# Kernel tuning notes

Hardware: AMD Instinct MI355X
Metric: run time of the kernel (lower is better)

Reference implementation:

```python
import jax, jax.numpy as jnp
import numpy as np

N_NODES = 100000
N_EDGES = 1600000
IN_DIM = 128
HID = 64
N_GRAPHS = 1024
EPS = 1e-5


def setup_inputs() -> dict:
    key = jax.random.key(0)
    ks = jax.random.split(key, 16)
    x = jax.random.normal(ks[0], (N_NODES, IN_DIM), dtype=jnp.float32)
    edge_index = jax.random.randint(ks[1], (2, N_EDGES), 0, N_NODES, dtype=jnp.int32)
    batch = jnp.sort(jax.random.randint(ks[2], (N_NODES,), 0, N_GRAPHS, dtype=jnp.int32))
    def glorot(k, shape):
        lim = np.sqrt(6.0 / (shape[0] + shape[1]))
        return jax.random.uniform(k, shape, jnp.float32, -lim, lim)
    return {
        'x': x, 'edge_index': edge_index, 'batch': batch,
        'w1': glorot(ks[3], (IN_DIM, HID)), 'b1': jnp.zeros((HID,), jnp.float32),
        'g1': jnp.ones((HID,), jnp.float32), 'be1': jnp.zeros((HID,), jnp.float32),
        'w2': glorot(ks[4], (HID, HID)), 'b2': jnp.zeros((HID,), jnp.float32),
        'g2': jnp.ones((HID,), jnp.float32), 'be2': jnp.zeros((HID,), jnp.float32),
        'w3': glorot(ks[5], (HID, HID)), 'b3': jnp.zeros((HID,), jnp.float32),
        'g3': jnp.ones((HID,), jnp.float32), 'be3': jnp.zeros((HID,), jnp.float32),
        'fc_w': glorot(ks[6], (HID, 1)), 'fc_b': jnp.zeros((1,), jnp.float32),
    }


def _batch_norm(h, gamma, beta):
    # training-mode BN over the node dimension (biased variance, as torch)
    mean = jnp.mean(h, axis=0)
    var = jnp.mean((h - mean) ** 2, axis=0)
    return (h - mean) * jax.lax.rsqrt(var + EPS) * gamma + beta


def reference(x, edge_index, batch, w1, b1, g1, be1, w2, b2, g2, be2,
              w3, b3, g3, be3, fc_w, fc_b):
    n = x.shape[0]
    # GCN normalization with added self-loops (PyG GCNConv semantics)
    loop = jnp.arange(n, dtype=edge_index.dtype)
    row = jnp.concatenate([edge_index[0], loop])  # source
    col = jnp.concatenate([edge_index[1], loop])  # target
    deg = jax.ops.segment_sum(jnp.ones_like(col, dtype=x.dtype), col, num_segments=n)
    dinv = jnp.where(deg > 0, jax.lax.rsqrt(deg), 0.0)
    norm = (dinv[row] * dinv[col])[:, None]  # [E+N, 1]

    def gcn(h, W, b):
        m = h @ W                                   # [N, HID]
        agg = jax.ops.segment_sum(m[row] * norm, col, num_segments=n)
        return agg + b

    h = jax.nn.relu(_batch_norm(gcn(x, w1, b1), g1, be1))
    res = h  # dropout is identity in eval mode
    h = jax.nn.relu(_batch_norm(gcn(h, w2, b2), g2, be2) + res)
    h = jax.nn.relu(_batch_norm(gcn(h, w3, b3), g3, be3))

    # global mean pool over graphs
    sums = jax.ops.segment_sum(h, batch, num_segments=N_GRAPHS)
    cnt = jax.ops.segment_sum(jnp.ones((n,), x.dtype), batch, num_segments=N_GRAPHS)
    pooled = sums / jnp.maximum(cnt, 1.0)[:, None]
    return (pooled @ fc_w + fc_b).squeeze(-1)  # [N_GRAPHS]
```

## Files before the change

kernel.cpp:

```cpp
#include <hip/hip_runtime.h>

#define NN 100000
#define NE 1600000
#define INDIM 128
#define HID 64
#define NG 1024
#define NB 1563
#define SCB 256
#define EPB ((NE + SCB - 1) / SCB)
#define SEGCAP 2048
#define BN_EPS 1e-5f

typedef unsigned short u16;
typedef unsigned int u32;

__device__ __forceinline__ u16 f2bf(float f) {
    u32 u = __float_as_uint(f);
    u32 r = (u + 0x7fffu + ((u >> 16) & 1u)) >> 16;
    return (u16)r;
}
__device__ __forceinline__ float bf2f(u32 b) {
    return __uint_as_float(b << 16);
}


__global__ void k_hist(const int* __restrict__ col, int* __restrict__ hist, int E) {
    __shared__ int h[NB];
    int b = blockIdx.x;
    for (int i = threadIdx.x; i < NB; i += 256) h[i] = 0;
    __syncthreads();
    int s = b * EPB, e = min(s + EPB, E);
    for (int i = s + threadIdx.x; i < e; i += 256) {
        atomicAdd(&h[col[i] >> 6], 1);
    }
    __syncthreads();
    for (int i = threadIdx.x; i < NB; i += 256) hist[b * NB + i] = h[i];
}

__global__ void k_btot(const int* __restrict__ hist, int* __restrict__ bcnt) {
    int t = blockIdx.x * 256 + threadIdx.x;
    if (t < NB) {
        int s = 0;
        for (int b = 0; b < SCB; b++) s += hist[b * NB + t];
        bcnt[t] = s;
    }
}

__global__ void k_bscan(const int* __restrict__ bcnt, int* __restrict__ bstart, int B, int E) {
    __shared__ int ts[256];
    int t = threadIdx.x;
    int loc[7];
    int s = 0;
    for (int i = 0; i < 7; i++) {
        int idx = t * 7 + i;
        loc[i] = (idx < B) ? bcnt[idx] : 0;
        s += loc[i];
    }
    ts[t] = s;
    __syncthreads();
    for (int off = 1; off < 256; off <<= 1) {
        int add = (t >= off) ? ts[t - off] : 0;
        __syncthreads();
        ts[t] += add;
        __syncthreads();
    }
    int ex = ts[t] - s;
    for (int i = 0; i < 7; i++) {
        int idx = t * 7 + i;
        if (idx < B) bstart[idx] = ex;
        ex += loc[i];
    }
    if (t == 0) bstart[B] = E;
}

__global__ void k_hcol(int* __restrict__ hist, const int* __restrict__ bstart) {
    int t = blockIdx.x * 256 + threadIdx.x;
    if (t < NB) {
        int run = bstart[t];
        for (int b = 0; b < SCB; b++) {
            int idx = b * NB + t;
            int v = hist[idx];
            hist[idx] = run;
            run += v;
        }
    }
}

__global__ void k_scatter(const int* __restrict__ row, const int* __restrict__ col,
                          const int* __restrict__ hist, u32* __restrict__ ebuf, int E) {
    __shared__ int cur[NB];
    int b = blockIdx.x;
    for (int i = threadIdx.x; i < NB; i += 256) cur[i] = hist[b * NB + i];
    __syncthreads();
    int s = b * EPB, e = min(s + EPB, E);
    for (int i = s + threadIdx.x; i < e; i += 256) {
        int c = col[i];
        int p = atomicAdd(&cur[c >> 6], 1);
        ebuf[p] = ((u32)row[i] << 6) | (u32)(c & 63);
    }
}

__global__ void k_degb(const u32* __restrict__ ebuf, const int* __restrict__ bstart,
                       float* __restrict__ dinv, int N) {
    __shared__ int lcnt[64];
    int b = blockIdx.x, t = threadIdx.x;
    if (t < 64) lcnt[t] = 0;
    __syncthreads();
    int s = bstart[b], e = bstart[b + 1];
    for (int i = s + t; i < e; i += 256) {
        atomicAdd(&lcnt[ebuf[i] & 63u], 1);
    }
    __syncthreads();
    if (t < 64) {
        int node = b * 64 + t;
        if (node < N) dinv[node] = rsqrtf((float)(lcnt[t] + 1));
    }
}


template<int K>
__global__ void k_gemm(const float* __restrict__ h, const float* __restrict__ W,
                       const float* __restrict__ dinv, u16* __restrict__ m, int N,
                       const float* __restrict__ bnStats, const float* __restrict__ bnG,
                       const float* __restrict__ bnB) {
    __shared__ float sh[16][K];
    const float invN = 1.0f / (float)N;
    const int K4 = K / 4;
    int block0 = blockIdx.x * 16;
    for (int idx = threadIdx.x; idx < 16 * K4; idx += 256) {
        int nn = idx / K4, kk4 = idx % K4;
        int node = block0 + nn;
        float4 v = make_float4(0.f, 0.f, 0.f, 0.f);
        if (node < N) v = *(const float4*)(h + (size_t)node * K + kk4 * 4);
        if (bnStats) {
            #pragma unroll
            for (int j = 0; j < 4; j++) {
                int kk = kk4 * 4 + j;
                float mean = bnStats[kk] * invN;
                float var = bnStats[K + kk] * invN - mean * mean;
                float sc = bnG[kk] * rsqrtf(var + BN_EPS);
                float* pv = (j == 0) ? &v.x : (j == 1) ? &v.y : (j == 2) ? &v.z : &v.w;
                *pv = fmaxf((*pv - mean) * sc + bnB[kk], 0.f);
            }
        }
        *(float4*)(&sh[nn][kk4 * 4]) = v;
    }
    __syncthreads();
    int colj = threadIdx.x & 63;
    int nl = threadIdx.x >> 6;
    float a0 = 0.f, a1 = 0.f, a2 = 0.f, a3 = 0.f;
    #pragma unroll 8
    for (int k = 0; k < K; k++) {
        float w = W[k * HID + colj];
        a0 += sh[nl][k] * w;
        a1 += sh[nl + 4][k] * w;
        a2 += sh[nl + 8][k] * w;
        a3 += sh[nl + 12][k] * w;
    }
    int n0 = block0 + nl;
    if (n0 < N)      m[(size_t)n0 * HID + colj]        = f2bf(a0 * dinv[n0]);
    if (n0 + 4 < N)  m[(size_t)(n0 + 4) * HID + colj]  = f2bf(a1 * dinv[n0 + 4]);
    if (n0 + 8 < N)  m[(size_t)(n0 + 8) * HID + colj]  = f2bf(a2 * dinv[n0 + 8]);
    if (n0 + 12 < N) m[(size_t)(n0 + 12) * HID + colj] = f2bf(a3 * dinv[n0 + 12]);
}

__global__ void k_gemm3(const float* __restrict__ agg1, const float* __restrict__ agg2,
                        const float* __restrict__ st1, const float* __restrict__ st2,
                        const float* __restrict__ g1, const float* __restrict__ be1,
                        const float* __restrict__ g2, const float* __restrict__ be2,
                        const float* __restrict__ W, const float* __restrict__ dinv,
                        u16* __restrict__ m, int N) {
    __shared__ float sh[16][HID];
    const float invN = 1.0f / (float)N;
    int block0 = blockIdx.x * 16;
    for (int idx = threadIdx.x; idx < 16 * 16; idx += 256) {
        int nn = idx / 16, kk4 = idx % 16;
        int node = block0 + nn;
        float4 o = make_float4(0.f, 0.f, 0.f, 0.f);
        if (node < N) {
            size_t p = (size_t)node * HID + kk4 * 4;
            float4 v1 = *(const float4*)(agg1 + p);
            float4 v2 = *(const float4*)(agg2 + p);
            float* p1 = &v1.x; float* p2 = &v2.x; float* po = &o.x;
            #pragma unroll
            for (int j = 0; j < 4; j++) {
                int kk = kk4 * 4 + j;
                float m1 = st1[kk] * invN;
                float va1 = st1[64 + kk] * invN - m1 * m1;
                float s1 = g1[kk] * rsqrtf(va1 + BN_EPS);
                float h1 = fmaxf((p1[j] - m1) * s1 + be1[kk], 0.f);
                float m2 = st2[kk] * invN;
                float va2 = st2[64 + kk] * invN - m2 * m2;
                float s2 = g2[kk] * rsqrtf(va2 + BN_EPS);
                po[j] = fmaxf((p2[j] - m2) * s2 + be2[kk] + h1, 0.f);
            }
        }
        *(float4*)(&sh[nn][kk4 * 4]) = o;
    }
    __syncthreads();
    int colj = threadIdx.x & 63;
    int nl = threadIdx.x >> 6;
    float a0 = 0.f, a1 = 0.f, a2 = 0.f, a3 = 0.f;
    #pragma unroll 8
    for (int k = 0; k < HID; k++) {
        float w = W[k * HID + colj];
        a0 += sh[nl][k] * w;
        a1 += sh[nl + 4][k] * w;
        a2 += sh[nl + 8][k] * w;
        a3 += sh[nl + 12][k] * w;
    }
    int n0 = block0 + nl;
    if (n0 < N)      m[(size_t)n0 * HID + colj]        = f2bf(a0 * dinv[n0]);
    if (n0 + 4 < N)  m[(size_t)(n0 + 4) * HID + colj]  = f2bf(a1 * dinv[n0 + 4]);
    if (n0 + 8 < N)  m[(size_t)(n0 + 8) * HID + colj]  = f2bf(a2 * dinv[n0 + 8]);
    if (n0 + 12 < N) m[(size_t)(n0 + 12) * HID + colj] = f2bf(a3 * dinv[n0 + 12]);
}

__global__ void __launch_bounds__(256)
k_fusedagg(const u16* __restrict__ m, const float* __restrict__ dinv,
           const u32* __restrict__ ebuf, const int* __restrict__ bstart,
           float* __restrict__ agg, float* __restrict__ stats, int N) {
    __shared__ u32 seg[SEGCAP];
    __shared__ u32 lrows[SEGCAP];
    __shared__ int lcnt[64], lstart[64], lcur[64];
    __shared__ float rs[4][64], rq[4][64];
    int b = blockIdx.x, t = threadIdx.x;
    int lane = t & 63, w = t >> 6;
    int s = bstart[b];
    int cnt = min(bstart[b + 1] - s, SEGCAP);
    if (t < 64) { lcnt[t] = 0; lcur[t] = 0; }
    __syncthreads();
    for (int i = t; i < cnt; i += 256) {
        u32 v = ebuf[s + i];
        seg[i] = v;
        atomicAdd(&lcnt[v & 63u], 1);
    }
    __syncthreads();
    if (w == 0) {
        int v = lcnt[lane];
        int x = v;
        for (int o = 1; o < 64; o <<= 1) {
            int y = __shfl_up(x, o, 64);
            if (lane >= o) x += y;
        }
        lstart[lane] = x - v;
    }
    __syncthreads();
    for (int i = t; i < cnt; i += 256) {
        u32 v = seg[i];
        int c = (int)(v & 63u);
        int p = lstart[c] + atomicAdd(&lcur[c], 1);
        lrows[p] = v >> 6;
    }
    __syncthreads();
    int node0 = b * 64;
    int g = lane >> 3;
    int sub = lane & 7;
    float ssum[8] = {0.f}, ssq[8] = {0.f};
    for (int i = 0; i < 16; i++) {
        int c = w * 16 + i;
        int node = node0 + c;
        if (node >= N) continue;
        float a[8] = {0.f, 0.f, 0.f, 0.f, 0.f, 0.f, 0.f, 0.f};
        if (g == 0) {
            uint4 v = ((const uint4*)(m + ((size_t)node << 6)))[sub];
            a[0] = bf2f(v.x & 0xffffu); a[1] = bf2f(v.x >> 16);
            a[2] = bf2f(v.y & 0xffffu); a[3] = bf2f(v.y >> 16);
            a[4] = bf2f(v.z & 0xffffu); a[5] = bf2f(v.z >> 16);
            a[6] = bf2f(v.w & 0xffffu); a[7] = bf2f(v.w >> 16);
        }
        int ls = lstart[c], cntc = lcnt[c];
        #pragma unroll 2
        for (int k = g; k < cntc; k += 8) {
            int r = (int)lrows[ls + k];
            uint4 v = ((const uint4*)(m + ((size_t)r << 6)))[sub];
            a[0] += bf2f(v.x & 0xffffu); a[1] += bf2f(v.x >> 16);
            a[2] += bf2f(v.y & 0xffffu); a[3] += bf2f(v.y >> 16);
            a[4] += bf2f(v.z & 0xffffu); a[5] += bf2f(v.z >> 16);
            a[6] += bf2f(v.w & 0xffffu); a[7] += bf2f(v.w >> 16);
        }
        #pragma unroll
        for (int j = 0; j < 8; j++) {
            a[j] += __shfl_xor(a[j], 8, 64);
            a[j] += __shfl_xor(a[j], 16, 64);
            a[j] += __shfl_xor(a[j], 32, 64);
        }
        if (lane < 8) {
            float di = dinv[node];
            float4 lo, hi;
            lo.x = a[0] * di; lo.y = a[1] * di; lo.z = a[2] * di; lo.w = a[3] * di;
            hi.x = a[4] * di; hi.y = a[5] * di; hi.z = a[6] * di; hi.w = a[7] * di;
            *(float4*)(agg + ((size_t)node << 6) + sub * 8)     = lo;
            *(float4*)(agg + ((size_t)node << 6) + sub * 8 + 4) = hi;
            ssum[0] += lo.x; ssum[1] += lo.y; ssum[2] += lo.z; ssum[3] += lo.w;
            ssum[4] += hi.x; ssum[5] += hi.y; ssum[6] += hi.z; ssum[7] += hi.w;
            ssq[0] += lo.x * lo.x; ssq[1] += lo.y * lo.y;
            ssq[2] += lo.z * lo.z; ssq[3] += lo.w * lo.w;
            ssq[4] += hi.x * hi.x; ssq[5] += hi.y * hi.y;
            ssq[6] += hi.z * hi.z; ssq[7] += hi.w * hi.w;
        }
    }
    if (lane < 8) {
        #pragma unroll
        for (int j = 0; j < 8; j++) {
            rs[w][sub * 8 + j] = ssum[j];
            rq[w][sub * 8 + j] = ssq[j];
        }
    }
    __syncthreads();
    if (w == 0) {
        float a = rs[0][lane] + rs[1][lane] + rs[2][lane] + rs[3][lane];
        float q = rq[0][lane] + rq[1][lane] + rq[2][lane] + rq[3][lane];
        atomicAdd(&stats[lane], a);
        atomicAdd(&stats[64 + lane], q);
    }
}

__global__ void k_pool(const float* __restrict__ agg3, const float* __restrict__ st3,
                       const float* __restrict__ g3, const float* __restrict__ be3,
                       const int* __restrict__ batch, float* __restrict__ pooled,
                       float* __restrict__ gcnt, int N) {
    int lane = threadIdx.x;
    int start = blockIdx.x * 64;
    if (start >= N) return;
    const float invN = 1.0f / (float)N;
    float mean = st3[lane] * invN;
    float var = st3[64 + lane] * invN - mean * mean;
    float sc = g3[lane] * rsqrtf(var + BN_EPS);
    float bb = be3[lane];
    int end = min(start + 64, N);
    int gcur = batch[start];
    float acc = 0.f; int run = 0;
    for (int n = start; n < end; n++) {
        int g = batch[n];
        if (g != gcur) {
            atomicAdd(&pooled[gcur * HID + lane], acc);
            if (lane == 0) atomicAdd(&gcnt[gcur], (float)run);
            acc = 0.f; run = 0; gcur = g;
        }
        acc += fmaxf((agg3[(size_t)n * HID + lane] - mean) * sc + bb, 0.f);
        run++;
    }
    atomicAdd(&pooled[gcur * HID + lane], acc);
    if (lane == 0) atomicAdd(&gcnt[gcur], (float)run);
}

__global__ void k_final(const float* __restrict__ pooled, const float* __restrict__ gcnt,
                        const float* __restrict__ fcw, const float* __restrict__ fcb,
                        float* __restrict__ out) {
    int g = (int)((blockIdx.x * (size_t)blockDim.x + threadIdx.x) >> 6);
    int lane = threadIdx.x & 63;
    if (g >= NG) return;
    float c = fmaxf(gcnt[g], 1.f);
    float v = pooled[g * HID + lane] / c * fcw[lane];
    for (int off = 32; off > 0; off >>= 1) v += __shfl_down(v, off, 64);
    if (lane == 0) out[g] = v + fcb[0];
}


extern "C" void kernel_launch(void* const* d_in, const int* in_sizes, int n_in,
                              void* d_out, int out_size, void* d_ws, size_t ws_size,
                              hipStream_t stream) {
    const float* x    = (const float*)d_in[0];
    const int*   ei   = (const int*)d_in[1];
    const int*   batch= (const int*)d_in[2];
    const float* w1   = (const float*)d_in[3];
    const float* g1   = (const float*)d_in[5];
    const float* be1  = (const float*)d_in[6];
    const float* w2   = (const float*)d_in[7];
    const float* g2   = (const float*)d_in[9];
    const float* be2  = (const float*)d_in[10];
    const float* w3   = (const float*)d_in[11];
    const float* g3   = (const float*)d_in[13];
    const float* be3  = (const float*)d_in[14];
    const float* fcw  = (const float*)d_in[15];
    const float* fcb  = (const float*)d_in[16];
    float* out = (float*)d_out;

    const int N = NN, E = NE;
    const int* erow = ei;
    const int* ecol = ei + E;

    char* ws = (char*)d_ws;
    size_t off = 0;
    auto alloc = [&](size_t bytes) -> char* {
        char* p = ws + off;
        off = (off + bytes + 255) & ~(size_t)255;
        return p;
    };
    float* dinv   = (float*)alloc((size_t)N * 4);
    int*   hist   = (int*)alloc((size_t)SCB * NB * 4);
    int*   bcnt   = (int*)alloc((size_t)NB * 4);
    int*   bstart = (int*)alloc((size_t)(NB + 1) * 4);
    u32*   ebuf   = (u32*)alloc((size_t)E * 4);
    u16*   bufM   = (u16*)alloc((size_t)N * HID * 2);
    float* aggB1  = (float*)alloc((size_t)N * HID * 4);
    float* aggB2  = (float*)alloc((size_t)N * HID * 4);
    float* stats  = (float*)alloc(3 * 128 * 4);
    float* pooled = (float*)alloc((size_t)NG * HID * 4);
    float* gcnt   = (float*)alloc((size_t)NG * 4);
    (void)ws_size; (void)in_sizes; (void)n_in; (void)out_size;

    float* aggB3 = aggB1;

    hipMemsetAsync(stats, 0, 3 * 128 * 4, stream);
    hipMemsetAsync(pooled, 0, (size_t)NG * HID * 4, stream);
    hipMemsetAsync(gcnt, 0, (size_t)NG * 4, stream);

    const int nbNode16 = (N + 15) / 16;
    const int nbB = (NB + 255) / 256;

    k_hist<<<SCB, 256, 0, stream>>>(ecol, hist, E);
    k_btot<<<nbB, 256, 0, stream>>>(hist, bcnt);
    k_bscan<<<1, 256, 0, stream>>>(bcnt, bstart, NB, E);
    k_hcol<<<nbB, 256, 0, stream>>>(hist, bstart);
    k_scatter<<<SCB, 256, 0, stream>>>(erow, ecol, hist, ebuf, E);
    k_degb<<<NB, 256, 0, stream>>>(ebuf, bstart, dinv, N);

    k_gemm<INDIM><<<nbNode16, 256, 0, stream>>>(x, w1, dinv, bufM, N,
                                                nullptr, nullptr, nullptr);
    k_fusedagg<<<NB, 256, 0, stream>>>(bufM, dinv, ebuf, bstart, aggB1, stats, N);

    k_gemm<HID><<<nbNode16, 256, 0, stream>>>(aggB1, w2, dinv, bufM, N,
                                              stats, g1, be1);
    k_fusedagg<<<NB, 256, 0, stream>>>(bufM, dinv, ebuf, bstart, aggB2, stats + 128, N);

    k_gemm3<<<nbNode16, 256, 0, stream>>>(aggB1, aggB2, stats, stats + 128,
                                          g1, be1, g2, be2, w3, dinv, bufM, N);
    k_fusedagg<<<NB, 256, 0, stream>>>(bufM, dinv, ebuf, bstart, aggB3, stats + 256, N);

    k_pool<<<(N + 63) / 64, 64, 0, stream>>>(aggB3, stats + 256, g3, be3,
                                             batch, pooled, gcnt, N);
    k_final<<<(NG * 64) / 256, 256, 0, stream>>>(pooled, gcnt, fcw, fcb, out);
}
```

Before: 503.2 us.

## Halve bucket size to 32 nodes and assign one 8-lane group per node

Measured after the change: 561.3 us. 11.6% more time.

```diff
diff --git a/kernel.cpp b/kernel.cpp
--- a/kernel.cpp
+++ b/kernel.cpp
@@ -5,10 +5,10 @@
 #define INDIM 128
 #define HID 64
 #define NG 1024
-#define NB 1563
+#define NB 3125
 #define SCB 256
 #define EPB ((NE + SCB - 1) / SCB)
-#define SEGCAP 2048
+#define SEGCAP 1024
 #define BN_EPS 1e-5f
 
 typedef unsigned short u16;
@@ -31,7 +31,7 @@
     __syncthreads();
     int s = b * EPB, e = min(s + EPB, E);
     for (int i = s + threadIdx.x; i < e; i += 256) {
-        atomicAdd(&h[col[i] >> 6], 1);
+        atomicAdd(&h[col[i] >> 5], 1);
     }
     __syncthreads();
     for (int i = threadIdx.x; i < NB; i += 256) hist[b * NB + i] = h[i];
@@ -49,10 +49,10 @@
 __global__ void k_bscan(const int* __restrict__ bcnt, int* __restrict__ bstart, int B, int E) {
     __shared__ int ts[256];
     int t = threadIdx.x;
-    int loc[7];
+    int loc[13];
     int s = 0;
-    for (int i = 0; i < 7; i++) {
-        int idx = t * 7 + i;
+    for (int i = 0; i < 13; i++) {
+        int idx = t * 13 + i;
         loc[i] = (idx < B) ? bcnt[idx] : 0;
         s += loc[i];
     }
@@ -65,8 +65,8 @@
         __syncthreads();
     }
     int ex = ts[t] - s;
-    for (int i = 0; i < 7; i++) {
-        int idx = t * 7 + i;
+    for (int i = 0; i < 13; i++) {
+        int idx = t * 13 + i;
         if (idx < B) bstart[idx] = ex;
         ex += loc[i];
     }
@@ -95,24 +95,24 @@
     int s = b * EPB, e = min(s + EPB, E);
     for (int i = s + threadIdx.x; i < e; i += 256) {
         int c = col[i];
-        int p = atomicAdd(&cur[c >> 6], 1);
-        ebuf[p] = ((u32)row[i] << 6) | (u32)(c & 63);
+        int p = atomicAdd(&cur[c >> 5], 1);
+        ebuf[p] = ((u32)row[i] << 5) | (u32)(c & 31);
     }
 }
 
 __global__ void k_degb(const u32* __restrict__ ebuf, const int* __restrict__ bstart,
                        float* __restrict__ dinv, int N) {
-    __shared__ int lcnt[64];
+    __shared__ int lcnt[32];
     int b = blockIdx.x, t = threadIdx.x;
-    if (t < 64) lcnt[t] = 0;
+    if (t < 32) lcnt[t] = 0;
     __syncthreads();
     int s = bstart[b], e = bstart[b + 1];
     for (int i = s + t; i < e; i += 256) {
-        atomicAdd(&lcnt[ebuf[i] & 63u], 1);
-    }
-    __syncthreads();
-    if (t < 64) {
-        int node = b * 64 + t;
+        atomicAdd(&lcnt[ebuf[i] & 31u], 1);
+    }
+    __syncthreads();
+    if (t < 32) {
+        int node = b * 32 + t;
         if (node < N) dinv[node] = rsqrtf((float)(lcnt[t] + 1));
     }
 }
@@ -220,91 +220,82 @@
 k_fusedagg(const u16* __restrict__ m, const float* __restrict__ dinv,
            const u32* __restrict__ ebuf, const int* __restrict__ bstart,
            float* __restrict__ agg, float* __restrict__ stats, int N) {
-    __shared__ u32 seg[SEGCAP];
     __shared__ u32 lrows[SEGCAP];
-    __shared__ int lcnt[64], lstart[64], lcur[64];
+    __shared__ int lcnt[32], lstart[32], lcur[32];
     __shared__ float rs[4][64], rq[4][64];
     int b = blockIdx.x, t = threadIdx.x;
     int lane = t & 63, w = t >> 6;
     int s = bstart[b];
     int cnt = min(bstart[b + 1] - s, SEGCAP);
-    if (t < 64) { lcnt[t] = 0; lcur[t] = 0; }
+    if (t < 32) { lcnt[t] = 0; lcur[t] = 0; }
+    __syncthreads();
+    for (int i = t; i < cnt; i += 256) {
+        atomicAdd(&lcnt[ebuf[s + i] & 31u], 1);
+    }
+    __syncthreads();
+    if (t < 64) {
+        int v = (lane < 32) ? lcnt[lane] : 0;
+        int x = v;
+        for (int o = 1; o < 32; o <<= 1) {
+            int y = __shfl_up(x, o, 64);
+            if (lane >= o) x += y;
+        }
+        if (lane < 32) lstart[lane] = x - v;
+    }
     __syncthreads();
     for (int i = t; i < cnt; i += 256) {
         u32 v = ebuf[s + i];
-        seg[i] = v;
-        atomicAdd(&lcnt[v & 63u], 1);
-    }
-    __syncthreads();
-    if (w == 0) {
-        int v = lcnt[lane];
-        int x = v;
-        for (int o = 1; o < 64; o <<= 1) {
-            int y = __shfl_up(x, o, 64);
-            if (lane >= o) x += y;
-        }
-        lstart[lane] = x - v;
-    }
-    __syncthreads();
-    for (int i = t; i < cnt; i += 256) {
-        u32 v = seg[i];
-        int c = (int)(v & 63u);
+        int c = (int)(v & 31u);
         int p = lstart[c] + atomicAdd(&lcur[c], 1);
-        lrows[p] = v >> 6;
-    }
-    __syncthreads();
-    int node0 = b * 64;
-    int g = lane >> 3;
-    int sub = lane & 7;
-    float ssum[8] = {0.f}, ssq[8] = {0.f};
-    for (int i = 0; i < 16; i++) {
-        int c = w * 16 + i;
-        int node = node0 + c;
-        if (node >= N) continue;
-        float a[8] = {0.f, 0.f, 0.f, 0.f, 0.f, 0.f, 0.f, 0.f};
-        if (g == 0) {
-            uint4 v = ((const uint4*)(m + ((size_t)node << 6)))[sub];
-            a[0] = bf2f(v.x & 0xffffu); a[1] = bf2f(v.x >> 16);
-            a[2] = bf2f(v.y & 0xffffu); a[3] = bf2f(v.y >> 16);
-            a[4] = bf2f(v.z & 0xffffu); a[5] = bf2f(v.z >> 16);
-            a[6] = bf2f(v.w & 0xffffu); a[7] = bf2f(v.w >> 16);
-        }
-        int ls = lstart[c], cntc = lcnt[c];
-        #pragma unroll 2
-        for (int k = g; k < cntc; k += 8) {
-            int r = (int)lrows[ls + k];
-            uint4 v = ((const uint4*)(m + ((size_t)r << 6)))[sub];
-            a[0] += bf2f(v.x & 0xffffu); a[1] += bf2f(v.x >> 16);
-            a[2] += bf2f(v.y & 0xffffu); a[3] += bf2f(v.y >> 16);
-            a[4] += bf2f(v.z & 0xffffu); a[5] += bf2f(v.z >> 16);
-            a[6] += bf2f(v.w & 0xffffu); a[7] += bf2f(v.w >> 16);
-        }
+        lrows[p] = v >> 5;
+    }
+    __syncthreads();
+    int grp = t >> 3;
+    int sub = t & 7;
+    int node = b * 32 + grp;
+    float val[8] = {0.f, 0.f, 0.f, 0.f, 0.f, 0.f, 0.f, 0.f};
+    if (node < N) {
+        float a[8];
+        uint4 v = ((const uint4*)(m + ((size_t)node << 6)))[sub];
+        a[0] = bf2f(v.x & 0xffffu); a[1] = bf2f(v.x >> 16);
+        a[2] = bf2f(v.y & 0xffffu); a[3] = bf2f(v.y >> 16);
+        a[4] = bf2f(v.z & 0xffffu); a[5] = bf2f(v.z >> 16);
+        a[6] = bf2f(v.w & 0xffffu); a[7] = bf2f(v.w >> 16);
+        int ls = lstart[grp], le = ls + lcnt[grp];
+        #pragma unroll 4
+        for (int j = ls; j < le; j++) {
+            int r = (int)lrows[j];
+            uint4 u = ((const uint4*)(m + ((size_t)r << 6)))[sub];
+            a[0] += bf2f(u.x & 0xffffu); a[1] += bf2f(u.x >> 16);
+            a[2] += bf2f(u.y & 0xffffu); a[3] += bf2f(u.y >> 16);
+            a[4] += bf2f(u.z & 0xffffu); a[5] += bf2f(u.z >> 16);
+            a[6] += bf2f(u.w & 0xffffu); a[7] += bf2f(u.w >> 16);
+        }
+        float di = dinv[node];
         #pragma unroll
-        for (int j = 0; j < 8; j++) {
-            a[j] += __shfl_xor(a[j], 8, 64);
-            a[j] += __shfl_xor(a[j], 16, 64);
-            a[j] += __shfl_xor(a[j], 32, 64);
-        }
-        if (lane < 8) {
-            float di = dinv[node];
-            float4 lo, hi;
-            lo.x = a[0] * di; lo.y = a[1] * di; lo.z = a[2] * di; lo.w = a[3] * di;
-            hi.x = a[4] * di; hi.y = a[5] * di; hi.z = a[6] * di; hi.w = a[7] * di;
-            *(float4*)(agg + ((size_t)node << 6) + sub * 8)     = lo;
-            *(float4*)(agg + ((size_t)node << 6) + sub * 8 + 4) = hi;
-            ssum[0] += lo.x; ssum[1] += lo.y; ssum[2] += lo.z; ssum[3] += lo.w;
-            ssum[4] += hi.x; ssum[5] += hi.y; ssum[6] += hi.z; ssum[7] += hi.w;
-            ssq[0] += lo.x * lo.x; ssq[1] += lo.y * lo.y;
-            ssq[2] += lo.z * lo.z; ssq[3] += lo.w * lo.w;
-            ssq[4] += hi.x * hi.x; ssq[5] += hi.y * hi.y;
-            ssq[6] += hi.z * hi.z; ssq[7] += hi.w * hi.w;
-        }
+        for (int j = 0; j < 8; j++) val[j] = a[j] * di;
+        float4 lo = make_float4(val[0], val[1], val[2], val[3]);
+        float4 hi = make_float4(val[4], val[5], val[6], val[7]);
+        *(float4*)(agg + ((size_t)node << 6) + sub * 8)     = lo;
+        *(float4*)(agg + ((size_t)node << 6) + sub * 8 + 4) = hi;
+    }
+    float sq[8];
+    #pragma unroll
+    for (int j = 0; j < 8; j++) sq[j] = val[j] * val[j];
+    #pragma unroll
+    for (int j = 0; j < 8; j++) {
+        val[j] += __shfl_xor(val[j], 8, 64);
+        val[j] += __shfl_xor(val[j], 16, 64);
+        val[j] += __shfl_xor(val[j], 32, 64);
+        sq[j]  += __shfl_xor(sq[j], 8, 64);
+        sq[j]  += __shfl_xor(sq[j], 16, 64);
+        sq[j]  += __shfl_xor(sq[j], 32, 64);
     }
     if (lane < 8) {
         #pragma unroll
         for (int j = 0; j < 8; j++) {
-            rs[w][sub * 8 + j] = ssum[j];
-            rq[w][sub * 8 + j] = ssq[j];
+            rs[w][sub * 8 + j] = val[j];
+            rq[w][sub * 8 + j] = sq[j];
         }
     }
     __syncthreads();
```

## Build global CSR once and split aggregation across two feature halves

Applied to the files above, without the earlier changes.

After: 605.4 us. 1.2x slower.

```diff
diff --git a/kernel.cpp b/kernel.cpp
--- a/kernel.cpp
+++ b/kernel.cpp
@@ -100,20 +100,48 @@
     }
 }
 
-__global__ void k_degb(const u32* __restrict__ ebuf, const int* __restrict__ bstart,
-                       float* __restrict__ dinv, int N) {
-    __shared__ int lcnt[64];
+__global__ void __launch_bounds__(256)
+k_csr(const u32* __restrict__ ebuf, const int* __restrict__ bstart,
+      u32* __restrict__ glrows, int* __restrict__ goffs,
+      float* __restrict__ dinv, int N) {
+    __shared__ u32 seg[SEGCAP];
+    __shared__ int lcnt[64], lstart[64], lcur[64];
     int b = blockIdx.x, t = threadIdx.x;
-    if (t < 64) lcnt[t] = 0;
-    __syncthreads();
-    int s = bstart[b], e = bstart[b + 1];
-    for (int i = s + t; i < e; i += 256) {
-        atomicAdd(&lcnt[ebuf[i] & 63u], 1);
-    }
-    __syncthreads();
+    int lane = t & 63, w = t >> 6;
+    int s = bstart[b];
+    int cnt = min(bstart[b + 1] - s, SEGCAP);
+    if (t < 64) { lcnt[t] = 0; lcur[t] = 0; }
+    __syncthreads();
+    for (int i = t; i < cnt; i += 256) {
+        u32 v = ebuf[s + i];
+        seg[i] = v;
+        atomicAdd(&lcnt[v & 63u], 1);
+    }
+    __syncthreads();
+    if (w == 0) {
+        int v = lcnt[lane];
+        int x = v;
+        for (int o = 1; o < 64; o <<= 1) {
+            int y = __shfl_up(x, o, 64);
+            if (lane >= o) x += y;
+        }
+        lstart[lane] = x - v;
+    }
+    __syncthreads();
+    for (int i = t; i < cnt; i += 256) {
+        u32 v = seg[i];
+        int c = (int)(v & 63u);
+        int p = s + lstart[c] + atomicAdd(&lcur[c], 1);
+        glrows[p] = v >> 6;
+    }
     if (t < 64) {
         int node = b * 64 + t;
-        if (node < N) dinv[node] = rsqrtf((float)(lcnt[t] + 1));
+        if (node < N) {
+            goffs[node] = s + lstart[t];
+            dinv[node] = rsqrtf((float)(lcnt[t] + 1));
+        } else if (node == N) {
+            goffs[N] = s + lstart[t];
+        }
     }
 }
 
@@ -218,101 +246,60 @@
 
 __global__ void __launch_bounds__(256)
 k_fusedagg(const u16* __restrict__ m, const float* __restrict__ dinv,
-           const u32* __restrict__ ebuf, const int* __restrict__ bstart,
+           const u32* __restrict__ glrows, const int* __restrict__ goffs,
            float* __restrict__ agg, float* __restrict__ stats, int N) {
-    __shared__ u32 seg[SEGCAP];
-    __shared__ u32 lrows[SEGCAP];
-    __shared__ int lcnt[64], lstart[64], lcur[64];
-    __shared__ float rs[4][64], rq[4][64];
-    int b = blockIdx.x, t = threadIdx.x;
+    __shared__ float rs[4][32], rq[4][32];
+    int b = blockIdx.x, hh = blockIdx.y;
+    int t = threadIdx.x;
     int lane = t & 63, w = t >> 6;
-    int s = bstart[b];
-    int cnt = min(bstart[b + 1] - s, SEGCAP);
-    if (t < 64) { lcnt[t] = 0; lcur[t] = 0; }
-    __syncthreads();
-    for (int i = t; i < cnt; i += 256) {
-        u32 v = ebuf[s + i];
-        seg[i] = v;
-        atomicAdd(&lcnt[v & 63u], 1);
-    }
-    __syncthreads();
-    if (w == 0) {
-        int v = lcnt[lane];
-        int x = v;
-        for (int o = 1; o < 64; o <<= 1) {
-            int y = __shfl_up(x, o, 64);
-            if (lane >= o) x += y;
-        }
-        lstart[lane] = x - v;
-    }
-    __syncthreads();
-    for (int i = t; i < cnt; i += 256) {
-        u32 v = seg[i];
-        int c = (int)(v & 63u);
-        int p = lstart[c] + atomicAdd(&lcur[c], 1);
-        lrows[p] = v >> 6;
-    }
-    __syncthreads();
-    int node0 = b * 64;
     int g = lane >> 3;
     int sub = lane & 7;
-    float ssum[8] = {0.f}, ssq[8] = {0.f};
+    int qidx = hh * 8 + sub;
+    int node0 = b * 64;
+    float ssum[4] = {0.f, 0.f, 0.f, 0.f}, ssq[4] = {0.f, 0.f, 0.f, 0.f};
     for (int i = 0; i < 16; i++) {
-        int c = w * 16 + i;
-        int node = node0 + c;
+        int node = node0 + w * 16 + i;
         if (node >= N) continue;
-        float a[8] = {0.f, 0.f, 0.f, 0.f, 0.f, 0.f, 0.f, 0.f};
+        float a0 = 0.f, a1 = 0.f, a2 = 0.f, a3 = 0.f;
         if (g == 0) {
-            uint4 v = ((const uint4*)(m + ((size_t)node << 6)))[sub];
-            a[0] = bf2f(v.x & 0xffffu); a[1] = bf2f(v.x >> 16);
-            a[2] = bf2f(v.y & 0xffffu); a[3] = bf2f(v.y >> 16);
-            a[4] = bf2f(v.z & 0xffffu); a[5] = bf2f(v.z >> 16);
-            a[6] = bf2f(v.w & 0xffffu); a[7] = bf2f(v.w >> 16);
-        }
-        int ls = lstart[c], cntc = lcnt[c];
+            uint2 v = ((const uint2*)(m + ((size_t)node << 6)))[qidx];
+            a0 = bf2f(v.x & 0xffffu); a1 = bf2f(v.x >> 16);
+            a2 = bf2f(v.y & 0xffffu); a3 = bf2f(v.y >> 16);
+        }
+        int s = goffs[node], e = goffs[node + 1];
         #pragma unroll 2
-        for (int k = g; k < cntc; k += 8) {
-            int r = (int)lrows[ls + k];
-            uint4 v = ((const uint4*)(m + ((size_t)r << 6)))[sub];
-            a[0] += bf2f(v.x & 0xffffu); a[1] += bf2f(v.x >> 16);
-            a[2] += bf2f(v.y & 0xffffu); a[3] += bf2f(v.y >> 16);
-            a[4] += bf2f(v.z & 0xffffu); a[5] += bf2f(v.z >> 16);
-            a[6] += bf2f(v.w & 0xffffu); a[7] += bf2f(v.w >> 16);
-        }
-        #pragma unroll
-        for (int j = 0; j < 8; j++) {
-            a[j] += __shfl_xor(a[j], 8, 64);
-            a[j] += __shfl_xor(a[j], 16, 64);
-            a[j] += __shfl_xor(a[j], 32, 64);
-        }
+        for (int k = s + g; k < e; k += 8) {
+            int r = (int)glrows[k];
+            uint2 v = ((const uint2*)(m + ((size_t)r << 6)))[qidx];
+            a0 += bf2f(v.x & 0xffffu); a1 += bf2f(v.x >> 16);
+            a2 += bf2f(v.y & 0xffffu); a3 += bf2f(v.y >> 16);
+        }
+        a0 += __shfl_xor(a0, 8, 64); a0 += __shfl_xor(a0, 16, 64); a0 += __shfl_xor(a0, 32, 64);
+        a1 += __shfl_xor(a1, 8, 64); a1 += __shfl_xor(a1, 16, 64); a1 += __shfl_xor(a1, 32, 64);
+        a2 += __shfl_xor(a2, 8, 64); a2 += __shfl_xor(a2, 16, 64); a2 += __shfl_xor(a2, 32, 64);
+        a3 += __shfl_xor(a3, 8, 64); a3 += __shfl_xor(a3, 16, 64); a3 += __shfl_xor(a3, 32, 64);
         if (lane < 8) {
             float di = dinv[node];
-            float4 lo, hi;
-            lo.x = a[0] * di; lo.y = a[1] * di; lo.z = a[2] * di; lo.w = a[3] * di;
-            hi.x = a[4] * di; hi.y = a[5] * di; hi.z = a[6] * di; hi.w = a[7] * di;
-            *(float4*)(agg + ((size_t)node << 6) + sub * 8)     = lo;
-            *(float4*)(agg + ((size_t)node << 6) + sub * 8 + 4) = hi;
-            ssum[0] += lo.x; ssum[1] += lo.y; ssum[2] += lo.z; ssum[3] += lo.w;
-            ssum[4] += hi.x; ssum[5] += hi.y; ssum[6] += hi.z; ssum[7] += hi.w;
-            ssq[0] += lo.x * lo.x; ssq[1] += lo.y * lo.y;
-            ssq[2] += lo.z * lo.z; ssq[3] += lo.w * lo.w;
-            ssq[4] += hi.x * hi.x; ssq[5] += hi.y * hi.y;
-            ssq[6] += hi.z * hi.z; ssq[7] += hi.w * hi.w;
+            float v0 = a0 * di, v1 = a1 * di, v2 = a2 * di, v3 = a3 * di;
+            *(float4*)(agg + ((size_t)node << 6) + hh * 32 + sub * 4) =
+                make_float4(v0, v1, v2, v3);
+            ssum[0] += v0; ssum[1] += v1; ssum[2] += v2; ssum[3] += v3;
+            ssq[0] += v0 * v0; ssq[1] += v1 * v1; ssq[2] += v2 * v2; ssq[3] += v3 * v3;
         }
     }
     if (lane < 8) {
         #pragma unroll
-        for (int j = 0; j < 8; j++) {
-            rs[w][sub * 8 + j] = ssum[j];
-            rq[w][sub * 8 + j] = ssq[j];
-        }
-    }
-    __syncthreads();
-    if (w == 0) {
+        for (int j = 0; j < 4; j++) {
+            rs[w][sub * 4 + j] = ssum[j];
+            rq[w][sub * 4 + j] = ssq[j];
+        }
+    }
+    __syncthreads();
+    if (w == 0 && lane < 32) {
         float a = rs[0][lane] + rs[1][lane] + rs[2][lane] + rs[3][lane];
         float q = rq[0][lane] + rq[1][lane] + rq[2][lane] + rq[3][lane];
-        atomicAdd(&stats[lane], a);
-        atomicAdd(&stats[64 + lane], q);
+        atomicAdd(&stats[hh * 32 + lane], a);
+        atomicAdd(&stats[64 + hh * 32 + lane], q);
     }
 }
 
@@ -393,6 +380,8 @@
     int*   bcnt   = (int*)alloc((size_t)NB * 4);
     int*   bstart = (int*)alloc((size_t)(NB + 1) * 4);
     u32*   ebuf   = (u32*)alloc((size_t)E * 4);
+    u32*   glrows = (u32*)alloc((size_t)E * 4);
+    int*   goffs  = (int*)alloc((size_t)(N + 1) * 4);
     u16*   bufM   = (u16*)alloc((size_t)N * HID * 2);
     float* aggB1  = (float*)alloc((size_t)N * HID * 4);
     float* aggB2  = (float*)alloc((size_t)N * HID * 4);
@@ -409,25 +398,26 @@
 
     const int nbNode16 = (N + 15) / 16;
     const int nbB = (NB + 255) / 256;
+    dim3 aggGrid(NB, 2);
 
     k_hist<<<SCB, 256, 0, stream>>>(ecol, hist, E);
     k_btot<<<nbB, 256, 0, stream>>>(hist, bcnt);
     k_bscan<<<1, 256, 0, stream>>>(bcnt, bstart, NB, E);
     k_hcol<<<nbB, 256, 0, stream>>>(hist, bstart);
     k_scatter<<<SCB, 256, 0, stream>>>(erow, ecol, hist, ebuf, E);
-    k_degb<<<NB, 256, 0, stream>>>(ebuf, bstart, dinv, N);
+    k_csr<<<NB, 256, 0, stream>>>(ebuf, bstart, glrows, goffs, dinv, N);
 
     k_gemm<INDIM><<<nbNode16, 256, 0, stream>>>(x, w1, dinv, bufM, N,
                                                 nullptr, nullptr, nullptr);
-    k_fusedagg<<<NB, 256, 0, stream>>>(bufM, dinv, ebuf, bstart, aggB1, stats, N);
+    k_fusedagg<<<aggGrid, 256, 0, stream>>>(bufM, dinv, glrows, goffs, aggB1, stats, N);
 
     k_gemm<HID><<<nbNode16, 256, 0, stream>>>(aggB1, w2, dinv, bufM, N,
                                               stats, g1, be1);
-    k_fusedagg<<<NB, 256, 0, stream>>>(bufM, dinv, ebuf, bstart, aggB2, stats + 128, N);
+    k_fusedagg<<<aggGrid, 256, 0, stream>>>(bufM, dinv, glrows, goffs, aggB2, stats + 128, N);
 
     k_gemm3<<<nbNode16, 256, 0, stream>>>(aggB1, aggB2, stats, stats + 128,
                                           g1, be1, g2, be2, w3, dinv, bufM, N);
-    k_fusedagg<<<NB, 256, 0, stream>>>(bufM, dinv, ebuf, bstart, aggB3, stats + 256, N);
+    k_fusedagg<<<aggGrid, 256, 0, stream>>>(bufM, dinv, glrows, goffs, aggB3, stats + 256, N);
 
     k_pool<<<(N + 63) / 64, 64, 0, stream>>>(aggB3, stats + 256, g3, be3,
                                              batch, pooled, gcnt, N);
```
